# Kernel tuning notes

Measured on AMD Instinct MI355X. Metric: run time of the kernel, lower is better.

The kernel has to match this reference:

```python
import jax, jax.numpy as jnp
import numpy as np

B, T, I, H = 256, 512, 256, 512


def setup_inputs() -> dict:
    key = jax.random.key(0)
    ks = jax.random.split(key, 7)
    s_ih = 1.0 / np.sqrt(I)
    s_hh = 1.0 / np.sqrt(H)
    return {
        "x": jax.random.normal(ks[0], (B, T, I), dtype=jnp.float32),
        "w_ih": jax.random.uniform(ks[1], (3 * H, I), jnp.float32, -s_ih, s_ih),
        "w_hh": jax.random.uniform(ks[2], (3 * H, H), jnp.float32, -s_hh, s_hh),
        "b": jax.random.uniform(ks[3], (3 * H,), jnp.float32, -s_hh, s_hh),
        "b_n": jax.random.uniform(ks[4], (H,), jnp.float32, -s_hh, s_hh),
        "w_proj": jax.random.uniform(ks[5], (1, H), jnp.float32, -s_hh, s_hh),
        "b_proj": jax.random.uniform(ks[6], (1,), jnp.float32, -s_hh, s_hh),
    }


def reference(x, w_ih, w_hh, b, b_n, w_proj, b_proj):
    # x: (B, T, I). Precompute all input-gate projections in one big GEMM.
    Bb, Tt, _ = x.shape
    Hh = w_hh.shape[1]
    igates = jnp.einsum("bti,gi->tbg", x, w_ih) + b  # (T, B, 3H)
    ir, iz, inn = jnp.split(igates, 3, axis=-1)  # each (T, B, H)

    def step(h, ig):
        ir_t, iz_t, in_t = ig
        hg = h @ w_hh.T  # (B, 3H)
        hr, hz, hn = jnp.split(hg, 3, axis=-1)
        r = jax.nn.sigmoid(ir_t + hr)
        z = jax.nn.sigmoid(iz_t + hz)
        n = jnp.tanh(in_t + r * (hn + b_n))
        # equinox GRUCell update: new + z * (hidden - new)
        h_new = n + z * (h - n)
        return h_new, None

    h0 = jnp.zeros((Bb, Hh), dtype=x.dtype)
    hT, _ = jax.lax.scan(step, h0, (ir, iz, inn))  # (B, H)
    e = hT @ w_proj.T + b_proj  # (B, 1)
    return jnp.squeeze(e, axis=-1)  # (B,)
```

## Files before the change

kernel.cpp:

```cpp
#include <hip/hip_runtime.h>
#include <stdint.h>

#define B_  256
#define T_  512
#define I_  256
#define H_  512
#define G3_ 1536

typedef _Float16 half8  __attribute__((ext_vector_type(8)));
typedef _Float16 half4v __attribute__((ext_vector_type(4)));
typedef float    float4v __attribute__((ext_vector_type(4)));

__device__ __forceinline__ float sigmoid_f(float x) { return 1.f / (1.f + __expf(-x)); }
__device__ __forceinline__ float tanh_f(float x) {
  x = fminf(15.f, fmaxf(-15.f, x));
  float e = __expf(2.f * x);
  return (e - 1.f) / (e + 1.f);
}

__global__ __launch_bounds__(256) void igates_gemm(
    const float* __restrict__ x, const float* __restrict__ w_ih,
    const float* __restrict__ bias, _Float16* __restrict__ ig)
{
  __shared__ _Float16 Ash[64][72];
  __shared__ _Float16 Bsh[64][72];
  const int tid  = threadIdx.x;
  const int lane = tid & 63;
  const int wv   = tid >> 6;
  const int wm   = wv >> 1, wn = wv & 1;
  const int n0   = blockIdx.x * 64;
  const int m0   = blockIdx.y * 64;

  float4v acc[2][2];
  #pragma unroll
  for (int a = 0; a < 2; ++a)
    #pragma unroll
    for (int c = 0; c < 2; ++c) acc[a][c] = (float4v){0.f, 0.f, 0.f, 0.f};

  for (int kc = 0; kc < I_; kc += 64) {
    #pragma unroll
    for (int i = 0; i < 4; ++i) {
      int e   = tid + (i << 8);
      int row = e >> 4;
      int c4  = e & 15;
      int m   = m0 + row;
      int tt  = m >> 8, bb = m & 255;
      float4 va = *(const float4*)(x + ((size_t)bb * T_ + tt) * I_ + kc + (c4 << 2));
      *(half4v*)&Ash[row][c4 << 2] =
          (half4v){(_Float16)va.x, (_Float16)va.y, (_Float16)va.z, (_Float16)va.w};
      float4 vb = *(const float4*)(w_ih + (size_t)(n0 + row) * I_ + kc + (c4 << 2));
      *(half4v*)&Bsh[row][c4 << 2] =
          (half4v){(_Float16)vb.x, (_Float16)vb.y, (_Float16)vb.z, (_Float16)vb.w};
    }
    __syncthreads();
    #pragma unroll
    for (int ks = 0; ks < 2; ++ks) {
      int kk = (ks << 5) + ((lane >> 4) << 3);
      half8 a0 = *(const half8*)&Ash[(wm << 5) + (lane & 15)][kk];
      half8 a1 = *(const half8*)&Ash[(wm << 5) + 16 + (lane & 15)][kk];
      half8 b0 = *(const half8*)&Bsh[(wn << 5) + (lane & 15)][kk];
      half8 b1 = *(const half8*)&Bsh[(wn << 5) + 16 + (lane & 15)][kk];
      acc[0][0] = __builtin_amdgcn_mfma_f32_16x16x32_f16(a0, b0, acc[0][0], 0, 0, 0);
      acc[0][1] = __builtin_amdgcn_mfma_f32_16x16x32_f16(a0, b1, acc[0][1], 0, 0, 0);
      acc[1][0] = __builtin_amdgcn_mfma_f32_16x16x32_f16(a1, b0, acc[1][0], 0, 0, 0);
      acc[1][1] = __builtin_amdgcn_mfma_f32_16x16x32_f16(a1, b1, acc[1][1], 0, 0, 0);
    }
    __syncthreads();
  }
  #pragma unroll
  for (int mt = 0; mt < 2; ++mt)
    #pragma unroll
    for (int nt = 0; nt < 2; ++nt) {
      int mrow = m0 + (wm << 5) + (mt << 4) + ((lane >> 4) << 2);
      int ncol = n0 + (wn << 5) + (nt << 4) + (lane & 15);
      float bb = bias[ncol];
      #pragma unroll
      for (int r = 0; r < 4; ++r)
        ig[(size_t)(mrow + r) * G3_ + ncol] = (_Float16)(acc[mt][nt][r] + bb);
    }
}

__global__ __launch_bounds__(256, 1) void gru_scan(
    const _Float16* __restrict__ ig, const float* __restrict__ w_hh,
    const float* __restrict__ b_n,
    _Float16* __restrict__ hb0, _Float16* __restrict__ hb1,
    int* flags)
{
  __shared__ _Float16 h_lds[16][520];
  __shared__ _Float16 hn_lds[16][74];

  const int tid   = threadIdx.x;
  const int lane  = tid & 63;
  const int wv    = tid >> 6;
  const int blk   = blockIdx.x;
  const int gb    = ((blk & 7) << 1) | ((blk >> 3) & 1);
  const int gs    = blk >> 4;
  const int b0    = gb << 4;
  const int j0    = gs << 6;
  const int jw    = j0 + (wv << 4);
  const int cn    = lane & 15;
  const int rquad = lane >> 4;

  half8 wfrag[3][16];
  #pragma unroll
  for (int g = 0; g < 3; ++g) {
    const float* wrow = w_hh + (size_t)(g * H_ + jw + cn) * H_;
    #pragma unroll
    for (int ks = 0; ks < 16; ++ks) {
      int k = (ks << 5) + (rquad << 3);
      half8 w;
      #pragma unroll
      for (int i = 0; i < 8; ++i) w[i] = (_Float16)wrow[k + i];
      wfrag[g][ks] = w;
    }
  }
  const float bnv = b_n[jw + cn];

  const int myflag = (gb << 3) | gs;
  _Float16* bufs[2] = { hb0, hb1 };

  for (int t = 0; t < T_; ++t) {
    float igv[3][4];
    {
      const _Float16* igb =
          ig + (size_t)(t * B_ + b0 + (rquad << 2)) * G3_ + jw + cn;
      #pragma unroll
      for (int g = 0; g < 3; ++g)
        #pragma unroll
        for (int r = 0; r < 4; ++r)
          igv[g][r] = (float)igb[(size_t)r * G3_ + g * H_];
    }

    if (t > 0) {
      if (tid < 8) {
        const int* fp = &flags[(gb << 3) | tid];
        while (__hip_atomic_load(fp, __ATOMIC_RELAXED,
                                 __HIP_MEMORY_SCOPE_AGENT) < t)
          __builtin_amdgcn_s_sleep(1);
      }
      __syncthreads();
    }

    const _Float16* hsrc = bufs[t & 1] + ((size_t)b0 << 9);
    {
      unsigned long long hv[8];
      #pragma unroll
      for (int i = 0; i < 8; ++i) {
        int idx = (i << 8) + tid;
        int row = idx >> 7, c = idx & 127;
        hv[i] = __hip_atomic_load(
            (const unsigned long long*)(hsrc + ((size_t)row << 9)) + c,
            __ATOMIC_RELAXED, __HIP_MEMORY_SCOPE_AGENT);
      }
      #pragma unroll
      for (int i = 0; i < 8; ++i) {
        int idx = (i << 8) + tid;
        int row = idx >> 7, c = idx & 127;
        *(unsigned long long*)&h_lds[row][c << 2] = hv[i];
      }
    }
    __syncthreads();

    float4v acc[3];
    acc[0] = (float4v){0.f, 0.f, 0.f, 0.f};
    acc[1] = (float4v){0.f, 0.f, 0.f, 0.f};
    acc[2] = (float4v){0.f, 0.f, 0.f, 0.f};
    #pragma unroll
    for (int ks = 0; ks < 16; ++ks) {
      half8 a = *(const half8*)&h_lds[cn][(ks << 5) + (rquad << 3)];
      acc[0] = __builtin_amdgcn_mfma_f32_16x16x32_f16(a, wfrag[0][ks], acc[0], 0, 0, 0);
      acc[1] = __builtin_amdgcn_mfma_f32_16x16x32_f16(a, wfrag[1][ks], acc[1], 0, 0, 0);
      acc[2] = __builtin_amdgcn_mfma_f32_16x16x32_f16(a, wfrag[2][ks], acc[2], 0, 0, 0);
    }

    #pragma unroll
    for (int r = 0; r < 4; ++r) {
      float rg = sigmoid_f(igv[0][r] + acc[0][r]);
      float zg = sigmoid_f(igv[1][r] + acc[1][r]);
      float nv = tanh_f(igv[2][r] + rg * (acc[2][r] + bnv));
      float hp = (float)h_lds[(rquad << 2) + r][jw + cn];
      hn_lds[(rquad << 2) + r][(wv << 4) + cn] = (_Float16)(nv + zg * (hp - nv));
    }
    __syncthreads();

    {
      int row = tid >> 4, c = tid & 15;
      unsigned long long v = *(const unsigned long long*)&hn_lds[row][c << 2];
      __hip_atomic_store(
          (unsigned long long*)(bufs[(t + 1) & 1] + (((size_t)(b0 + row)) << 9) + j0) + c,
          v, __ATOMIC_RELAXED, __HIP_MEMORY_SCOPE_AGENT);
    }
    __builtin_amdgcn_s_waitcnt(0);
    __syncthreads();
    if (tid == 0)
      __hip_atomic_store(&flags[myflag], t + 1,
                         __ATOMIC_RELAXED, __HIP_MEMORY_SCOPE_AGENT);
  }
}

__global__ __launch_bounds__(64) void proj_kernel(
    const _Float16* __restrict__ h, const float* __restrict__ w_proj,
    const float* __restrict__ b_proj, float* __restrict__ out)
{
  int b = blockIdx.x;
  int lane = threadIdx.x;
  float s = 0.f;
  #pragma unroll
  for (int i = 0; i < 8; ++i) {
    int j = lane + (i << 6);
    s += (float)h[((size_t)b << 9) + j] * w_proj[j];
  }
  #pragma unroll
  for (int off = 32; off > 0; off >>= 1) s += __shfl_down(s, off, 64);
  if (lane == 0) out[b] = s + b_proj[0];
}

extern "C" void kernel_launch(void* const* d_in, const int* in_sizes, int n_in,
                              void* d_out, int out_size, void* d_ws, size_t ws_size,
                              hipStream_t stream) {
  const float* x      = (const float*)d_in[0];
  const float* w_ih   = (const float*)d_in[1];
  const float* w_hh   = (const float*)d_in[2];
  const float* bias   = (const float*)d_in[3];
  const float* b_n    = (const float*)d_in[4];
  const float* w_proj = (const float*)d_in[5];
  const float* b_proj = (const float*)d_in[6];
  float* out = (float*)d_out;

  char* ws = (char*)d_ws;
  const size_t IG_BYTES = (size_t)T_ * B_ * G3_ * sizeof(_Float16);
  const size_t HB_BYTES = (size_t)B_ * H_ * sizeof(_Float16);
  _Float16* igbuf = (_Float16*)ws;
  _Float16* hbuf0 = (_Float16*)(ws + IG_BYTES);
  _Float16* hbuf1 = (_Float16*)(ws + IG_BYTES + HB_BYTES);
  int*      flags = (int*)(ws + IG_BYTES + 2 * HB_BYTES);

  hipMemsetAsync(ws + IG_BYTES, 0, 2 * HB_BYTES + 1024, stream);

  dim3 gridA(G3_ / 64, (T_ * B_) / 64);
  igates_gemm<<<gridA, 256, 0, stream>>>(x, w_ih, bias, igbuf);
  gru_scan<<<128, 256, 0, stream>>>(igbuf, w_hh, b_n, hbuf0, hbuf1, flags);
  proj_kernel<<<B_, 64, 0, stream>>>(hbuf0, w_proj, b_proj, out);
}
```

Before: 2.177 ms.

## Replace per-step flag barrier with tagged hidden-state words and enlarge GEMM tiles

The scan kernel drops its separate flag array and spin-wait barrier. Each fp16 hidden value is now stored in a 32-bit word whose upper half holds the step index, and consumers poll the data words directly until every tag matches, which removes the flag store/load round trip and two block barriers per step. The input-gate GEMM moves to 128x128 tiles with a 4x4 MFMA block per wave and packed fp16 conversion, and the recurrent MFMA chain is split into two accumulators to shorten dependencies. The cost is twice the hidden-state traffic, plus reliance on per-word atomicity for correctness. Only buffer 0 is zeroed, which works because step 0 expects tag 0.

New measurement: 2.563 ms. 17.7% more time.

```diff
diff --git a/kernel.cpp b/kernel.cpp
--- a/kernel.cpp
+++ b/kernel.cpp
@@ -9,6 +9,7 @@
 
 typedef _Float16 half8  __attribute__((ext_vector_type(8)));
 typedef _Float16 half4v __attribute__((ext_vector_type(4)));
+typedef __fp16   fp16x2 __attribute__((ext_vector_type(2)));
 typedef float    float4v __attribute__((ext_vector_type(4)));
 
 __device__ __forceinline__ float sigmoid_f(float x) { return 1.f / (1.f + __expf(-x)); }
@@ -18,88 +19,99 @@
   return (e - 1.f) / (e + 1.f);
 }
 
+__device__ __forceinline__ unsigned pk2(float lo, float hi) {
+  fp16x2 p = __builtin_amdgcn_cvt_pkrtz(lo, hi);
+  return *(unsigned*)&p;
+}
+
 __global__ __launch_bounds__(256) void igates_gemm(
     const float* __restrict__ x, const float* __restrict__ w_ih,
     const float* __restrict__ bias, _Float16* __restrict__ ig)
 {
-  __shared__ _Float16 Ash[64][72];
-  __shared__ _Float16 Bsh[64][72];
+  __shared__ _Float16 Ash[128][72];
+  __shared__ _Float16 Bsh[128][72];
   const int tid  = threadIdx.x;
   const int lane = tid & 63;
   const int wv   = tid >> 6;
   const int wm   = wv >> 1, wn = wv & 1;
-  const int n0   = blockIdx.x * 64;
-  const int m0   = blockIdx.y * 64;
-
-  float4v acc[2][2];
-  #pragma unroll
-  for (int a = 0; a < 2; ++a)
-    #pragma unroll
-    for (int c = 0; c < 2; ++c) acc[a][c] = (float4v){0.f, 0.f, 0.f, 0.f};
+  const int n0   = blockIdx.x * 128;
+  const int m0   = blockIdx.y * 128;
+  const int cn   = lane & 15;
+  const int rq   = lane >> 4;
+
+  float4v acc[4][4];
+  #pragma unroll
+  for (int a = 0; a < 4; ++a)
+    #pragma unroll
+    for (int c = 0; c < 4; ++c) acc[a][c] = (float4v){0.f, 0.f, 0.f, 0.f};
 
   for (int kc = 0; kc < I_; kc += 64) {
     #pragma unroll
-    for (int i = 0; i < 4; ++i) {
+    for (int i = 0; i < 8; ++i) {
       int e   = tid + (i << 8);
       int row = e >> 4;
       int c4  = e & 15;
       int m   = m0 + row;
       int tt  = m >> 8, bb = m & 255;
       float4 va = *(const float4*)(x + ((size_t)bb * T_ + tt) * I_ + kc + (c4 << 2));
-      *(half4v*)&Ash[row][c4 << 2] =
-          (half4v){(_Float16)va.x, (_Float16)va.y, (_Float16)va.z, (_Float16)va.w};
+      uint2 ua; ua.x = pk2(va.x, va.y); ua.y = pk2(va.z, va.w);
+      *(uint2*)&Ash[row][c4 << 2] = ua;
       float4 vb = *(const float4*)(w_ih + (size_t)(n0 + row) * I_ + kc + (c4 << 2));
-      *(half4v*)&Bsh[row][c4 << 2] =
-          (half4v){(_Float16)vb.x, (_Float16)vb.y, (_Float16)vb.z, (_Float16)vb.w};
+      uint2 ub; ub.x = pk2(vb.x, vb.y); ub.y = pk2(vb.z, vb.w);
+      *(uint2*)&Bsh[row][c4 << 2] = ub;
     }
     __syncthreads();
     #pragma unroll
     for (int ks = 0; ks < 2; ++ks) {
-      int kk = (ks << 5) + ((lane >> 4) << 3);
-      half8 a0 = *(const half8*)&Ash[(wm << 5) + (lane & 15)][kk];
-      half8 a1 = *(const half8*)&Ash[(wm << 5) + 16 + (lane & 15)][kk];
-      half8 b0 = *(const half8*)&Bsh[(wn << 5) + (lane & 15)][kk];
-      half8 b1 = *(const half8*)&Bsh[(wn << 5) + 16 + (lane & 15)][kk];
-      acc[0][0] = __builtin_amdgcn_mfma_f32_16x16x32_f16(a0, b0, acc[0][0], 0, 0, 0);
-      acc[0][1] = __builtin_amdgcn_mfma_f32_16x16x32_f16(a0, b1, acc[0][1], 0, 0, 0);
-      acc[1][0] = __builtin_amdgcn_mfma_f32_16x16x32_f16(a1, b0, acc[1][0], 0, 0, 0);
-      acc[1][1] = __builtin_amdgcn_mfma_f32_16x16x32_f16(a1, b1, acc[1][1], 0, 0, 0);
-    }
-    __syncthreads();
-  }
-  #pragma unroll
-  for (int mt = 0; mt < 2; ++mt)
-    #pragma unroll
-    for (int nt = 0; nt < 2; ++nt) {
-      int mrow = m0 + (wm << 5) + (mt << 4) + ((lane >> 4) << 2);
-      int ncol = n0 + (wn << 5) + (nt << 4) + (lane & 15);
-      float bb = bias[ncol];
+      int kk = (ks << 5) + (rq << 3);
+      half8 af[4], bf[4];
+      #pragma unroll
+      for (int mt = 0; mt < 4; ++mt)
+        af[mt] = *(const half8*)&Ash[(wm << 6) + (mt << 4) + cn][kk];
+      #pragma unroll
+      for (int nt = 0; nt < 4; ++nt)
+        bf[nt] = *(const half8*)&Bsh[(wn << 6) + (nt << 4) + cn][kk];
+      #pragma unroll
+      for (int mt = 0; mt < 4; ++mt)
+        #pragma unroll
+        for (int nt = 0; nt < 4; ++nt)
+          acc[mt][nt] = __builtin_amdgcn_mfma_f32_16x16x32_f16(af[mt], bf[nt], acc[mt][nt], 0, 0, 0);
+    }
+    __syncthreads();
+  }
+  float bv[4];
+  #pragma unroll
+  for (int nt = 0; nt < 4; ++nt) bv[nt] = bias[n0 + (wn << 6) + (nt << 4) + cn];
+  #pragma unroll
+  for (int mt = 0; mt < 4; ++mt)
+    #pragma unroll
+    for (int nt = 0; nt < 4; ++nt) {
+      int mrow = m0 + (wm << 6) + (mt << 4) + (rq << 2);
+      int ncol = n0 + (wn << 6) + (nt << 4) + cn;
       #pragma unroll
       for (int r = 0; r < 4; ++r)
-        ig[(size_t)(mrow + r) * G3_ + ncol] = (_Float16)(acc[mt][nt][r] + bb);
+        ig[(size_t)(mrow + r) * G3_ + ncol] = (_Float16)(acc[mt][nt][r] + bv[nt]);
     }
 }
 
 __global__ __launch_bounds__(256, 1) void gru_scan(
     const _Float16* __restrict__ ig, const float* __restrict__ w_hh,
     const float* __restrict__ b_n,
-    _Float16* __restrict__ hb0, _Float16* __restrict__ hb1,
-    int* flags)
+    uint32_t* __restrict__ hb0, uint32_t* __restrict__ hb1)
 {
   __shared__ _Float16 h_lds[16][520];
-  __shared__ _Float16 hn_lds[16][74];
-
-  const int tid   = threadIdx.x;
-  const int lane  = tid & 63;
-  const int wv    = tid >> 6;
-  const int blk   = blockIdx.x;
-  const int gb    = ((blk & 7) << 1) | ((blk >> 3) & 1);
-  const int gs    = blk >> 4;
-  const int b0    = gb << 4;
-  const int j0    = gs << 6;
-  const int jw    = j0 + (wv << 4);
-  const int cn    = lane & 15;
-  const int rquad = lane >> 4;
+
+  const int tid  = threadIdx.x;
+  const int lane = tid & 63;
+  const int wv   = tid >> 6;
+  const int blk  = blockIdx.x;
+  const int gb   = ((blk & 7) << 1) | ((blk >> 3) & 1);
+  const int gs   = blk >> 4;
+  const int b0   = gb << 4;
+  const int j0   = gs << 6;
+  const int jw   = j0 + (wv << 4);
+  const int cn   = lane & 15;
+  const int rq   = lane >> 4;
 
   half8 wfrag[3][16];
   #pragma unroll
@@ -107,7 +119,7 @@
     const float* wrow = w_hh + (size_t)(g * H_ + jw + cn) * H_;
     #pragma unroll
     for (int ks = 0; ks < 16; ++ks) {
-      int k = (ks << 5) + (rquad << 3);
+      int k = (ks << 5) + (rq << 3);
       half8 w;
       #pragma unroll
       for (int i = 0; i < 8; ++i) w[i] = (_Float16)wrow[k + i];
@@ -116,14 +128,20 @@
   }
   const float bnv = b_n[jw + cn];
 
-  const int myflag = (gb << 3) | gs;
-  _Float16* bufs[2] = { hb0, hb1 };
+  uint32_t* bufs[2] = { hb0, hb1 };
 
   for (int t = 0; t < T_; ++t) {
+    const uint64_t* src = (const uint64_t*)bufs[t & 1] + ((size_t)b0 << 8);
+    uint64_t hv[16];
+    #pragma unroll
+    for (int i = 0; i < 16; ++i)
+      hv[i] = __hip_atomic_load(src + (i << 8) + tid,
+                                __ATOMIC_RELAXED, __HIP_MEMORY_SCOPE_AGENT);
+
     float igv[3][4];
     {
       const _Float16* igb =
-          ig + (size_t)(t * B_ + b0 + (rquad << 2)) * G3_ + jw + cn;
+          ig + (size_t)(t * B_ + b0 + (rq << 2)) * G3_ + jw + cn;
       #pragma unroll
       for (int g = 0; g < 3; ++g)
         #pragma unroll
@@ -131,75 +149,66 @@
           igv[g][r] = (float)igb[(size_t)r * G3_ + g * H_];
     }
 
-    if (t > 0) {
-      if (tid < 8) {
-        const int* fp = &flags[(gb << 3) | tid];
-        while (__hip_atomic_load(fp, __ATOMIC_RELAXED,
-                                 __HIP_MEMORY_SCOPE_AGENT) < t)
-          __builtin_amdgcn_s_sleep(1);
-      }
-      __syncthreads();
-    }
-
-    const _Float16* hsrc = bufs[t & 1] + ((size_t)b0 << 9);
-    {
-      unsigned long long hv[8];
-      #pragma unroll
-      for (int i = 0; i < 8; ++i) {
-        int idx = (i << 8) + tid;
-        int row = idx >> 7, c = idx & 127;
-        hv[i] = __hip_atomic_load(
-            (const unsigned long long*)(hsrc + ((size_t)row << 9)) + c,
-            __ATOMIC_RELAXED, __HIP_MEMORY_SCOPE_AGENT);
-      }
-      #pragma unroll
-      for (int i = 0; i < 8; ++i) {
-        int idx = (i << 8) + tid;
-        int row = idx >> 7, c = idx & 127;
-        *(unsigned long long*)&h_lds[row][c << 2] = hv[i];
-      }
-    }
-    __syncthreads();
-
-    float4v acc[3];
-    acc[0] = (float4v){0.f, 0.f, 0.f, 0.f};
-    acc[1] = (float4v){0.f, 0.f, 0.f, 0.f};
-    acc[2] = (float4v){0.f, 0.f, 0.f, 0.f};
+    const uint64_t patt = ((uint64_t)(uint32_t)t << 16) | ((uint64_t)(uint32_t)t << 48);
+    uint32_t pend = 0;
+    #pragma unroll
+    for (int i = 0; i < 16; ++i)
+      if ((hv[i] & 0xFFFF0000FFFF0000ULL) != patt) pend |= (1u << i);
+    while (pend) {
+      #pragma unroll
+      for (int i = 0; i < 16; ++i)
+        if (pend & (1u << i))
+          hv[i] = __hip_atomic_load(src + (i << 8) + tid,
+                                    __ATOMIC_RELAXED, __HIP_MEMORY_SCOPE_AGENT);
+      #pragma unroll
+      for (int i = 0; i < 16; ++i)
+        if ((pend & (1u << i)) && (hv[i] & 0xFFFF0000FFFF0000ULL) == patt)
+          pend &= ~(1u << i);
+    }
+
+    #pragma unroll
+    for (int i = 0; i < 16; ++i) {
+      int idx = (i << 8) + tid;
+      int row = idx >> 8, cp = idx & 255;
+      uint32_t pk = (uint32_t)(hv[i] & 0xFFFF) | ((uint32_t)(hv[i] >> 32) << 16);
+      *(uint32_t*)&h_lds[row][cp << 1] = pk;
+    }
+    __syncthreads();
+
+    float4v acc[3][2];
+    #pragma unroll
+    for (int g = 0; g < 3; ++g) {
+      acc[g][0] = (float4v){0.f, 0.f, 0.f, 0.f};
+      acc[g][1] = (float4v){0.f, 0.f, 0.f, 0.f};
+    }
     #pragma unroll
     for (int ks = 0; ks < 16; ++ks) {
-      half8 a = *(const half8*)&h_lds[cn][(ks << 5) + (rquad << 3)];
-      acc[0] = __builtin_amdgcn_mfma_f32_16x16x32_f16(a, wfrag[0][ks], acc[0], 0, 0, 0);
-      acc[1] = __builtin_amdgcn_mfma_f32_16x16x32_f16(a, wfrag[1][ks], acc[1], 0, 0, 0);
-      acc[2] = __builtin_amdgcn_mfma_f32_16x16x32_f16(a, wfrag[2][ks], acc[2], 0, 0, 0);
-    }
-
+      half8 a = *(const half8*)&h_lds[cn][(ks << 5) + (rq << 3)];
+      int p = ks & 1;
+      acc[0][p] = __builtin_amdgcn_mfma_f32_16x16x32_f16(a, wfrag[0][ks], acc[0][p], 0, 0, 0);
+      acc[1][p] = __builtin_amdgcn_mfma_f32_16x16x32_f16(a, wfrag[1][ks], acc[1][p], 0, 0, 0);
+      acc[2][p] = __builtin_amdgcn_mfma_f32_16x16x32_f16(a, wfrag[2][ks], acc[2][p], 0, 0, 0);
+    }
+
+    uint32_t* dst = bufs[(t + 1) & 1];
+    const uint32_t tagbits = (uint32_t)(t + 1) << 16;
     #pragma unroll
     for (int r = 0; r < 4; ++r) {
-      float rg = sigmoid_f(igv[0][r] + acc[0][r]);
-      float zg = sigmoid_f(igv[1][r] + acc[1][r]);
-      float nv = tanh_f(igv[2][r] + rg * (acc[2][r] + bnv));
-      float hp = (float)h_lds[(rquad << 2) + r][jw + cn];
-      hn_lds[(rquad << 2) + r][(wv << 4) + cn] = (_Float16)(nv + zg * (hp - nv));
-    }
-    __syncthreads();
-
-    {
-      int row = tid >> 4, c = tid & 15;
-      unsigned long long v = *(const unsigned long long*)&hn_lds[row][c << 2];
-      __hip_atomic_store(
-          (unsigned long long*)(bufs[(t + 1) & 1] + (((size_t)(b0 + row)) << 9) + j0) + c,
-          v, __ATOMIC_RELAXED, __HIP_MEMORY_SCOPE_AGENT);
-    }
-    __builtin_amdgcn_s_waitcnt(0);
-    __syncthreads();
-    if (tid == 0)
-      __hip_atomic_store(&flags[myflag], t + 1,
-                         __ATOMIC_RELAXED, __HIP_MEMORY_SCOPE_AGENT);
+      float rg = sigmoid_f(igv[0][r] + acc[0][0][r] + acc[0][1][r]);
+      float zg = sigmoid_f(igv[1][r] + acc[1][0][r] + acc[1][1][r]);
+      float nv = tanh_f(igv[2][r] + rg * (acc[2][0][r] + acc[2][1][r] + bnv));
+      float hp = (float)h_lds[(rq << 2) + r][jw + cn];
+      _Float16 hh = (_Float16)(nv + zg * (hp - nv));
+      uint32_t val = tagbits | (uint32_t)*(uint16_t*)&hh;
+      __hip_atomic_store(dst + (((size_t)(b0 + (rq << 2) + r)) << 9) + jw + cn,
+                         val, __ATOMIC_RELAXED, __HIP_MEMORY_SCOPE_AGENT);
+    }
+    __syncthreads();
   }
 }
 
 __global__ __launch_bounds__(64) void proj_kernel(
-    const _Float16* __restrict__ h, const float* __restrict__ w_proj,
+    const uint32_t* __restrict__ h, const float* __restrict__ w_proj,
     const float* __restrict__ b_proj, float* __restrict__ out)
 {
   int b = blockIdx.x;
@@ -208,7 +217,8 @@
   #pragma unroll
   for (int i = 0; i < 8; ++i) {
     int j = lane + (i << 6);
-    s += (float)h[((size_t)b << 9) + j] * w_proj[j];
+    uint16_t u = (uint16_t)(h[((size_t)b << 9) + j] & 0xFFFF);
+    s += (float)*(_Float16*)&u * w_proj[j];
   }
   #pragma unroll
   for (int off = 32; off > 0; off >>= 1) s += __shfl_down(s, off, 64);
@@ -229,16 +239,15 @@
 
   char* ws = (char*)d_ws;
   const size_t IG_BYTES = (size_t)T_ * B_ * G3_ * sizeof(_Float16);
-  const size_t HB_BYTES = (size_t)B_ * H_ * sizeof(_Float16);
+  const size_t HB_BYTES = (size_t)B_ * H_ * sizeof(uint32_t);
   _Float16* igbuf = (_Float16*)ws;
-  _Float16* hbuf0 = (_Float16*)(ws + IG_BYTES);
-  _Float16* hbuf1 = (_Float16*)(ws + IG_BYTES + HB_BYTES);
-  int*      flags = (int*)(ws + IG_BYTES + 2 * HB_BYTES);
-
-  hipMemsetAsync(ws + IG_BYTES, 0, 2 * HB_BYTES + 1024, stream);
-
-  dim3 gridA(G3_ / 64, (T_ * B_) / 64);
+  uint32_t* hbuf0 = (uint32_t*)(ws + IG_BYTES);
+  uint32_t* hbuf1 = (uint32_t*)(ws + IG_BYTES + HB_BYTES);
+
+  (void)hipMemsetAsync(ws + IG_BYTES, 0, HB_BYTES, stream);
+
+  dim3 gridA(G3_ / 128, (T_ * B_) / 128);
   igates_gemm<<<gridA, 256, 0, stream>>>(x, w_ih, bias, igbuf);
-  gru_scan<<<128, 256, 0, stream>>>(igbuf, w_hh, b_n, hbuf0, hbuf1, flags);
+  gru_scan<<<128, 256, 0, stream>>>(igbuf, w_hh, b_n, hbuf0, hbuf1);
   proj_kernel<<<B_, 64, 0, stream>>>(hbuf0, w_proj, b_proj, out);
 }
```
